# Optimization experiments

Hardware: AMD Instinct MI355X
Metric: run time of the kernel (lower is better)

## Reference

```python
import jax, jax.numpy as jnp
import numpy as np

B, S, E, H = 4, 2048, 1024, 16
DK = E // H  # 64


def setup_inputs() -> dict:
    key = jax.random.key(0)
    ks = jax.random.split(key, 6)
    scale = 1.0 / np.sqrt(E)
    return {
        "x": jax.random.normal(ks[0], (B, S, E), dtype=jnp.float32),
        "Wq": jax.random.normal(ks[1], (E, E), dtype=jnp.float32) * scale,
        "Wk": jax.random.normal(ks[2], (E, E), dtype=jnp.float32) * scale,
        "Wv": jax.random.normal(ks[3], (E, E), dtype=jnp.float32) * scale,
        "Wo": jax.random.normal(ks[4], (E, E), dtype=jnp.float32) * scale,
        "theta": jax.random.normal(ks[5], (DK,), dtype=jnp.float32),
    }


def _heads(t):
    # [B,S,E] -> [B,H,S,DK]
    b, s, _ = t.shape
    return t.reshape(b, s, H, DK).transpose(0, 2, 1, 3)


def reference(x, Wq, Wk, Wv, Wo, theta):
    # nn.Linear (no bias): y = x @ W.T
    # quantum transform: independent single-qubit RX(x)->RX(theta)->  <Z> = cos(x+theta)
    q = jnp.cos(_heads(x @ Wq.T) + theta)  # [B,H,S,DK]
    k = jnp.cos(_heads(x @ Wk.T) + theta)
    v = jnp.cos(_heads(x @ Wv.T) + theta)
    scores = jnp.einsum("bhqd,bhkd->bhqk", q, k) / jnp.sqrt(jnp.float32(DK))
    attn = jax.nn.softmax(scores, axis=-1)  # dropout is identity in eval
    out = jnp.einsum("bhqk,bhkd->bhqd", attn, v)  # [B,H,S,DK]
    out = out.transpose(0, 2, 1, 3).reshape(x.shape[0], -1, E)
    return out @ Wo.T
```

## Files before the change

### kernel.cpp

```cpp
#include <hip/hip_runtime.h>

#define B_  4
#define S_  2048
#define E_  1024
#define H_  16
#define DK_ 64
#define M_  (B_*S_)

typedef __attribute__((ext_vector_type(8)))  short short8;
typedef __attribute__((ext_vector_type(4)))  float f32x4;
typedef __attribute__((ext_vector_type(16))) float f32x16;

#define QSCALE 0.18033688f

__device__ __forceinline__ unsigned short f2b(float f) {
    union { float f; unsigned u; } v; v.f = f;
    unsigned u = v.u;
    return (unsigned short)((u + 0x7fffu + ((u >> 16) & 1u)) >> 16);
}

__device__ __forceinline__ void gload_lds16(const unsigned short* g, unsigned short* l) {
    __builtin_amdgcn_global_load_lds((const __attribute__((address_space(1))) void*)g,
                                     (__attribute__((address_space(3))) void*)l, 16, 0, 0);
}

__global__ __launch_bounds__(256) void cvt_x(const float* __restrict__ src,
                                             unsigned short* __restrict__ dst) {
    int i = blockIdx.x * 256 + threadIdx.x;
    float4 f = ((const float4*)src)[i];
    ushort4 o;
    o.x = f2b(f.x); o.y = f2b(f.y); o.z = f2b(f.z); o.w = f2b(f.w);
    ((ushort4*)dst)[i] = o;
}

__global__ __launch_bounds__(256) void cvt_w(const float* __restrict__ w0, const float* __restrict__ w1,
                                             const float* __restrict__ w2, const float* __restrict__ w3,
                                             unsigned short* __restrict__ wb,
                                             unsigned short* __restrict__ wob) {
    int z = blockIdx.y;
    const float* src = (z == 0) ? w0 : (z == 1) ? w1 : (z == 2) ? w2 : w3;
    unsigned short* dst = (z < 3) ? wb + (size_t)z * E_ * E_ : wob;
    int i = blockIdx.x * 256 + threadIdx.x;
    float4 f = ((const float4*)src)[i];
    ushort4 o;
    o.x = f2b(f.x); o.y = f2b(f.y); o.z = f2b(f.z); o.w = f2b(f.w);
    ((ushort4*)dst)[i] = o;
}

__global__ __launch_bounds__(256) void gemm_qkv(
    const unsigned short* __restrict__ xb,
    const unsigned short* __restrict__ Wb,
    const float* __restrict__ theta,
    unsigned short* __restrict__ qb,
    unsigned short* __restrict__ kb,
    unsigned short* __restrict__ vtb)
{
    __shared__ unsigned short smem[128*144];
    unsigned short* As = smem;
    unsigned short* Bs = smem + 128*64;
    const int tid = threadIdx.x;
    const int w = tid >> 6, lane = tid & 63, quad = lane >> 4, col = lane & 15;
    const int wm = (w & 1) * 64, wn = (w >> 1) * 64;
    const int m0 = blockIdx.x * 128, n0 = blockIdx.y * 128, z = blockIdx.z;
    const unsigned short* Wz = Wb + (size_t)z * E_ * E_;
    const int srow = lane >> 3, schunk = (lane & 7) * 8;

    f32x4 acc[4][4] = {};
    for (int k0 = 0; k0 < E_; k0 += 64) {
        #pragma unroll
        for (int c = 0; c < 4; c++) {
            int row = w*32 + c*8 + srow;
            gload_lds16(&xb[(size_t)(m0+row)*E_ + k0 + schunk], &As[(w*32 + c*8)*64]);
            gload_lds16(&Wz[(size_t)(n0+row)*E_ + k0 + schunk], &Bs[(w*32 + c*8)*64]);
        }
        __syncthreads();
        #pragma unroll
        for (int kk = 0; kk < 64; kk += 32) {
            short8 a[4], b[4];
            #pragma unroll
            for (int i = 0; i < 4; i++)
                a[i] = *(const short8*)&As[(wm + i*16 + col)*64 + kk + quad*8];
            #pragma unroll
            for (int j = 0; j < 4; j++)
                b[j] = *(const short8*)&Bs[(wn + j*16 + col)*64 + kk + quad*8];
            #pragma unroll
            for (int i = 0; i < 4; i++)
                #pragma unroll
                for (int j = 0; j < 4; j++)
                    acc[i][j] = __builtin_amdgcn_mfma_f32_16x16x32_bf16(a[i], b[j], acc[i][j], 0, 0, 0);
        }
        __syncthreads();
    }

    const int bblk = m0 >> 11;
    const int sbase = m0 & (S_-1);

    if (z != 2) {
        const float qs = (z == 0) ? QSCALE : 1.0f;
        #pragma unroll
        for (int j = 0; j < 4; j++) {
            int nl = wn + j*16 + col;
            float th = theta[(n0 + nl) & 63];
            #pragma unroll
            for (int i = 0; i < 4; i++)
                #pragma unroll
                for (int r = 0; r < 4; r++) {
                    int ml = wm + i*16 + quad*4 + r;
                    int nls = nl ^ (((ml >> 2) & 3) << 4);
                    smem[ml*144 + nls] = f2b(__cosf(acc[i][j][r] + th) * qs);
                }
        }
        __syncthreads();
        unsigned short* dst = (z == 0) ? qb : kb;
        const int h0 = n0 >> 6;
        #pragma unroll
        for (int k = 0; k < 8; k++) {
            int idx = k*256 + tid;
            int chunk = idx & 7, seg = idx >> 3;
            int ml = seg >> 1, hh = seg & 1;
            int ch = chunk ^ (((ml >> 2) & 3) << 1);
            int4 val = *(const int4*)&smem[ml*144 + hh*64 + ch*8];
            size_t g = ((size_t)(bblk*H_ + h0 + hh)*S_ + sbase + ml)*DK_ + chunk*8;
            *(int4*)&dst[g] = val;
        }
    } else {
        #pragma unroll
        for (int j = 0; j < 4; j++) {
            int nl = wn + j*16 + col;
            float th = theta[(n0 + nl) & 63];
            #pragma unroll
            for (int i = 0; i < 4; i++)
                #pragma unroll
                for (int r = 0; r < 4; r++)
                    smem[nl*136 + wm + i*16 + quad*4 + r] = f2b(__cosf(acc[i][j][r] + th));
        }
        __syncthreads();
        int row = tid >> 1, halfm = (tid & 1) * 64;
        int n = n0 + row, h = n >> 6, d = n & 63;
        size_t base = ((size_t)(bblk*H_ + h)*DK_ + d)*S_ + sbase + halfm;
        #pragma unroll
        for (int k = 0; k < 8; k++)
            *(int4*)&vtb[base + k*8] = *(const int4*)&smem[row*136 + halfm + k*8];
    }
}

__global__ __launch_bounds__(256) void gemm_out(
    const unsigned short* __restrict__ ctx,
    const unsigned short* __restrict__ Wob,
    float* __restrict__ out)
{
    __shared__ unsigned short As[128*64];
    __shared__ unsigned short Bs[128*64];
    const int tid = threadIdx.x;
    const int w = tid >> 6, lane = tid & 63, quad = lane >> 4, col = lane & 15;
    const int wm = (w & 1) * 64, wn = (w >> 1) * 64;
    const int m0 = blockIdx.x * 128, n0 = blockIdx.y * 128;
    const int srow = lane >> 3, schunk = (lane & 7) * 8;

    f32x4 acc[4][4] = {};
    for (int k0 = 0; k0 < E_; k0 += 64) {
        #pragma unroll
        for (int c = 0; c < 4; c++) {
            int row = w*32 + c*8 + srow;
            gload_lds16(&ctx[(size_t)(m0+row)*E_ + k0 + schunk], &As[(w*32 + c*8)*64]);
            gload_lds16(&Wob[(size_t)(n0+row)*E_ + k0 + schunk], &Bs[(w*32 + c*8)*64]);
        }
        __syncthreads();
        #pragma unroll
        for (int kk = 0; kk < 64; kk += 32) {
            short8 a[4], b[4];
            #pragma unroll
            for (int i = 0; i < 4; i++)
                a[i] = *(const short8*)&As[(wm + i*16 + col)*64 + kk + quad*8];
            #pragma unroll
            for (int j = 0; j < 4; j++)
                b[j] = *(const short8*)&Bs[(wn + j*16 + col)*64 + kk + quad*8];
            #pragma unroll
            for (int i = 0; i < 4; i++)
                #pragma unroll
                for (int j = 0; j < 4; j++)
                    acc[i][j] = __builtin_amdgcn_mfma_f32_16x16x32_bf16(a[i], b[j], acc[i][j], 0, 0, 0);
        }
        __syncthreads();
    }
    #pragma unroll
    for (int j = 0; j < 4; j++) {
        int n = n0 + wn + j*16 + col;
        #pragma unroll
        for (int i = 0; i < 4; i++)
            #pragma unroll
            for (int r = 0; r < 4; r++) {
                int m = m0 + wm + i*16 + quad*4 + r;
                out[(size_t)m*E_ + n] = acc[i][j][r];
            }
    }
}

#define LPK 72

__global__ __launch_bounds__(256, 4) void flash_attn(
    const unsigned short* __restrict__ qb,
    const unsigned short* __restrict__ kb,
    const unsigned short* __restrict__ vtb,
    unsigned short* __restrict__ ctx)
{
    __shared__ unsigned short Kt[64*LPK];
    __shared__ unsigned short Vt[64*LPK];
    const int tid = threadIdx.x;
    const int w = tid >> 6, lane = tid & 63, col = lane & 31, half = lane >> 5;
    const int q0 = blockIdx.x * 128;
    const int bh = blockIdx.y;

    short8 qf[4];
    {
        const unsigned short* qrow = qb + ((size_t)bh*S_ + q0 + w*32 + col)*DK_;
        #pragma unroll
        for (int c = 0; c < 4; c++)
            qf[c] = *(const short8*)&qrow[c*16 + half*8];
    }

    union U8 { unsigned u[4]; short8 s8; };
    U8 ones;
    #pragma unroll
    for (int i = 0; i < 4; i++) ones.u[i] = 0x3F803F80u;

    f32x16 oacc[2] = {};
    f32x16 lacc = {};

    for (int kt = 0; kt < S_; kt += 64) {
        __syncthreads();
        for (int i = tid; i < 512; i += 256) {
            int row = i >> 3, c8 = (i & 7) * 8;
            *(int4*)&Kt[row*LPK + c8] = *(const int4*)&kb [((size_t)bh*S_  + kt + row)*DK_ + c8];
            *(int4*)&Vt[row*LPK + c8] = *(const int4*)&vtb[((size_t)bh*DK_ + row)*S_ + kt + c8];
        }
        __syncthreads();

        #pragma unroll
        for (int t = 0; t < 2; t++) {
            f32x16 sacc = {};
            #pragma unroll
            for (int c = 0; c < 4; c++) {
                short8 kf = *(const short8*)&Kt[(t*32 + col)*LPK + c*16 + half*8];
                sacc = __builtin_amdgcn_mfma_f32_32x32x16_bf16(kf, qf[c], sacc, 0, 0, 0);
            }
            unsigned pk[4][2], pp[4][2];
            #pragma unroll
            for (int rg = 0; rg < 4; rg++) {
                float p0 = __builtin_amdgcn_exp2f(sacc[rg*4+0]);
                float p1 = __builtin_amdgcn_exp2f(sacc[rg*4+1]);
                float p2 = __builtin_amdgcn_exp2f(sacc[rg*4+2]);
                float p3 = __builtin_amdgcn_exp2f(sacc[rg*4+3]);
                pk[rg][0] = (__float_as_uint(p0) >> 16) | (__float_as_uint(p1) & 0xffff0000u);
                pk[rg][1] = (__float_as_uint(p2) >> 16) | (__float_as_uint(p3) & 0xffff0000u);
            }
            #pragma unroll
            for (int rg = 0; rg < 4; rg++) {
                pp[rg][0] = __shfl_xor((int)pk[rg][0], 32);
                pp[rg][1] = __shfl_xor((int)pk[rg][1], 32);
            }
            #pragma unroll
            for (int kc = 0; kc < 2; kc++) {
                const int lo = 2*kc, hi = 2*kc + 1;
                U8 pa;
                pa.u[0] = half ? pp[hi][0] : pk[lo][0];
                pa.u[1] = half ? pp[hi][1] : pk[lo][1];
                pa.u[2] = half ? pk[hi][0] : pp[lo][0];
                pa.u[3] = half ? pk[hi][1] : pp[lo][1];
                lacc = __builtin_amdgcn_mfma_f32_32x32x16_bf16(pa.s8, ones.s8, lacc, 0, 0, 0);
                #pragma unroll
                for (int dt = 0; dt < 2; dt++) {
                    short8 vf = *(const short8*)&Vt[(dt*32 + col)*LPK + t*32 + kc*16 + half*8];
                    oacc[dt] = __builtin_amdgcn_mfma_f32_32x32x16_bf16(pa.s8, vf, oacc[dt], 0, 0, 0);
                }
            }
        }
    }

    const int b = bh >> 4, h = bh & 15;
    #pragma unroll
    for (int rg = 0; rg < 4; rg++)
        #pragma unroll
        for (int rr = 0; rr < 4; rr++) {
            int row = rr + rg*8 + half*4;
            float inv = 1.0f / lacc[rg*4 + rr];
            int s = q0 + w*32 + row;
            size_t rowoff = ((size_t)(b*S_ + s))*E_ + h*64;
            #pragma unroll
            for (int dt = 0; dt < 2; dt++)
                ctx[rowoff + dt*32 + col] = f2b(oacc[dt][rg*4 + rr] * inv);
        }
}

extern "C" void kernel_launch(void* const* d_in, const int* in_sizes, int n_in,
                              void* d_out, int out_size, void* d_ws, size_t ws_size,
                              hipStream_t stream) {
    (void)in_sizes; (void)n_in; (void)out_size; (void)ws_size;
    const float* x     = (const float*)d_in[0];
    const float* Wq    = (const float*)d_in[1];
    const float* Wk    = (const float*)d_in[2];
    const float* Wv    = (const float*)d_in[3];
    const float* Wo    = (const float*)d_in[4];
    const float* theta = (const float*)d_in[5];
    float* out = (float*)d_out;

    unsigned short* ws  = (unsigned short*)d_ws;
    unsigned short* xb  = ws;
    unsigned short* Wb  = xb  + (size_t)M_*E_;
    unsigned short* Wob = Wb  + (size_t)3*E_*E_;
    unsigned short* qb  = Wob + (size_t)E_*E_;
    unsigned short* kb  = qb  + (size_t)B_*H_*S_*DK_;
    unsigned short* vtb = kb  + (size_t)B_*H_*S_*DK_;
    unsigned short* ctx = xb;

    cvt_x<<<M_*E_/4/256, 256, 0, stream>>>(x, xb);
    cvt_w<<<dim3(E_*E_/4/256, 4), 256, 0, stream>>>(Wq, Wk, Wv, Wo, Wb, Wob);

    gemm_qkv<<<dim3(M_/128, E_/128, 3), 256, 0, stream>>>(xb, Wb, theta, qb, kb, vtb);
    flash_attn<<<dim3(S_/128, B_*H_), 256, 0, stream>>>(qb, kb, vtb, ctx);
    gemm_out<<<dim3(M_/128, E_/128), 256, 0, stream>>>(ctx, Wob, out);
}
```

Measured before the change: 295.7 us.

## Double query rows per attention wave and replace row-sum MFMA with VALU sums

Each attention wave now handles two 32-row query groups, reusing the K and V fragments loaded from LDS across both groups and halving the number of blocks. The softmax denominator is accumulated with plain adds and a cross-half shuffle instead of an extra MFMA against a ones matrix, and bf16 packing uses byte-permute with fewer shuffles. The separate x and weight conversion kernels are merged into a single launch. In exchange, register pressure rises, the occupancy hint drops from 4 to 2 blocks, and fewer blocks are available to fill the GPU.

```diff
diff --git a/kernel.cpp b/kernel.cpp
--- a/kernel.cpp
+++ b/kernel.cpp
@@ -24,27 +24,30 @@
                                      (__attribute__((address_space(3))) void*)l, 16, 0, 0);
 }
 
-__global__ __launch_bounds__(256) void cvt_x(const float* __restrict__ src,
-                                             unsigned short* __restrict__ dst) {
+#define XN4 (M_*E_/4)
+#define WN4 (E_*E_/4)
+__global__ __launch_bounds__(256) void cvt_all(
+    const float* __restrict__ x,
+    const float* __restrict__ w0, const float* __restrict__ w1,
+    const float* __restrict__ w2, const float* __restrict__ w3,
+    unsigned short* __restrict__ xb, unsigned short* __restrict__ wb,
+    unsigned short* __restrict__ wob) {
     int i = blockIdx.x * 256 + threadIdx.x;
-    float4 f = ((const float4*)src)[i];
+    const float* src;
+    unsigned short* dst;
+    int idx;
+    if (i < XN4) { src = x; dst = xb; idx = i; }
+    else {
+        int j = i - XN4;
+        int z = j >> 18;
+        idx = j & (WN4 - 1);
+        src = (z == 0) ? w0 : (z == 1) ? w1 : (z == 2) ? w2 : w3;
+        dst = (z < 3) ? wb + (size_t)z * E_ * E_ : wob;
+    }
+    float4 f = ((const float4*)src)[idx];
     ushort4 o;
     o.x = f2b(f.x); o.y = f2b(f.y); o.z = f2b(f.z); o.w = f2b(f.w);
-    ((ushort4*)dst)[i] = o;
-}
-
-__global__ __launch_bounds__(256) void cvt_w(const float* __restrict__ w0, const float* __restrict__ w1,
-                                             const float* __restrict__ w2, const float* __restrict__ w3,
-                                             unsigned short* __restrict__ wb,
-                                             unsigned short* __restrict__ wob) {
-    int z = blockIdx.y;
-    const float* src = (z == 0) ? w0 : (z == 1) ? w1 : (z == 2) ? w2 : w3;
-    unsigned short* dst = (z < 3) ? wb + (size_t)z * E_ * E_ : wob;
-    int i = blockIdx.x * 256 + threadIdx.x;
-    float4 f = ((const float4*)src)[i];
-    ushort4 o;
-    o.x = f2b(f.x); o.y = f2b(f.y); o.z = f2b(f.z); o.w = f2b(f.w);
-    ((ushort4*)dst)[i] = o;
+    ((ushort4*)dst)[idx] = o;
 }
 
 __global__ __launch_bounds__(256) void gemm_qkv(
@@ -198,7 +201,7 @@
 
 #define LPK 72
 
-__global__ __launch_bounds__(256, 4) void flash_attn(
+__global__ __launch_bounds__(256, 2) void flash_attn(
     const unsigned short* __restrict__ qb,
     const unsigned short* __restrict__ kb,
     const unsigned short* __restrict__ vtb,
@@ -208,24 +211,22 @@
     __shared__ unsigned short Vt[64*LPK];
     const int tid = threadIdx.x;
     const int w = tid >> 6, lane = tid & 63, col = lane & 31, half = lane >> 5;
-    const int q0 = blockIdx.x * 128;
+    const int q0 = blockIdx.x * 256;
     const int bh = blockIdx.y;
 
-    short8 qf[4];
-    {
-        const unsigned short* qrow = qb + ((size_t)bh*S_ + q0 + w*32 + col)*DK_;
+    union U8 { unsigned u[4]; short8 s8; };
+
+    short8 qf[2][4];
+    #pragma unroll
+    for (int qg = 0; qg < 2; qg++) {
+        const unsigned short* qrow = qb + ((size_t)bh*S_ + q0 + w*64 + qg*32 + col)*DK_;
         #pragma unroll
         for (int c = 0; c < 4; c++)
-            qf[c] = *(const short8*)&qrow[c*16 + half*8];
-    }
-
-    union U8 { unsigned u[4]; short8 s8; };
-    U8 ones;
-    #pragma unroll
-    for (int i = 0; i < 4; i++) ones.u[i] = 0x3F803F80u;
-
-    f32x16 oacc[2] = {};
-    f32x16 lacc = {};
+            qf[qg][c] = *(const short8*)&qrow[c*16 + half*8];
+    }
+
+    float rsum[2] = {0.f, 0.f};
+    f32x16 oacc[2][2] = {};
 
     for (int kt = 0; kt < S_; kt += 64) {
         __syncthreads();
@@ -238,40 +239,49 @@
 
         #pragma unroll
         for (int t = 0; t < 2; t++) {
-            f32x16 sacc = {};
-            #pragma unroll
-            for (int c = 0; c < 4; c++) {
-                short8 kf = *(const short8*)&Kt[(t*32 + col)*LPK + c*16 + half*8];
-                sacc = __builtin_amdgcn_mfma_f32_32x32x16_bf16(kf, qf[c], sacc, 0, 0, 0);
-            }
-            unsigned pk[4][2], pp[4][2];
-            #pragma unroll
-            for (int rg = 0; rg < 4; rg++) {
-                float p0 = __builtin_amdgcn_exp2f(sacc[rg*4+0]);
-                float p1 = __builtin_amdgcn_exp2f(sacc[rg*4+1]);
-                float p2 = __builtin_amdgcn_exp2f(sacc[rg*4+2]);
-                float p3 = __builtin_amdgcn_exp2f(sacc[rg*4+3]);
-                pk[rg][0] = (__float_as_uint(p0) >> 16) | (__float_as_uint(p1) & 0xffff0000u);
-                pk[rg][1] = (__float_as_uint(p2) >> 16) | (__float_as_uint(p3) & 0xffff0000u);
-            }
-            #pragma unroll
-            for (int rg = 0; rg < 4; rg++) {
-                pp[rg][0] = __shfl_xor((int)pk[rg][0], 32);
-                pp[rg][1] = __shfl_xor((int)pk[rg][1], 32);
-            }
-            #pragma unroll
-            for (int kc = 0; kc < 2; kc++) {
-                const int lo = 2*kc, hi = 2*kc + 1;
-                U8 pa;
-                pa.u[0] = half ? pp[hi][0] : pk[lo][0];
-                pa.u[1] = half ? pp[hi][1] : pk[lo][1];
-                pa.u[2] = half ? pk[hi][0] : pp[lo][0];
-                pa.u[3] = half ? pk[hi][1] : pp[lo][1];
-                lacc = __builtin_amdgcn_mfma_f32_32x32x16_bf16(pa.s8, ones.s8, lacc, 0, 0, 0);
-                #pragma unroll
-                for (int dt = 0; dt < 2; dt++) {
-                    short8 vf = *(const short8*)&Vt[(dt*32 + col)*LPK + t*32 + kc*16 + half*8];
-                    oacc[dt] = __builtin_amdgcn_mfma_f32_32x32x16_bf16(pa.s8, vf, oacc[dt], 0, 0, 0);
+            short8 kf[4];
+            #pragma unroll
+            for (int c = 0; c < 4; c++)
+                kf[c] = *(const short8*)&Kt[(t*32 + col)*LPK + c*16 + half*8];
+            short8 vf[2][2];
+            #pragma unroll
+            for (int kc = 0; kc < 2; kc++)
+                #pragma unroll
+                for (int dt = 0; dt < 2; dt++)
+                    vf[kc][dt] = *(const short8*)&Vt[(dt*32 + col)*LPK + t*32 + kc*16 + half*8];
+
+            #pragma unroll
+            for (int qg = 0; qg < 2; qg++) {
+                f32x16 sacc = {};
+                #pragma unroll
+                for (int c = 0; c < 4; c++)
+                    sacc = __builtin_amdgcn_mfma_f32_32x32x16_bf16(kf[c], qf[qg][c], sacc, 0, 0, 0);
+                unsigned pk[4][2];
+                #pragma unroll
+                for (int rg = 0; rg < 4; rg++) {
+                    float p0 = __builtin_amdgcn_exp2f(sacc[rg*4+0]);
+                    float p1 = __builtin_amdgcn_exp2f(sacc[rg*4+1]);
+                    float p2 = __builtin_amdgcn_exp2f(sacc[rg*4+2]);
+                    float p3 = __builtin_amdgcn_exp2f(sacc[rg*4+3]);
+                    rsum[qg] += (p0 + p1) + (p2 + p3);
+                    pk[rg][0] = __builtin_amdgcn_perm(__float_as_uint(p1), __float_as_uint(p0), 0x07060302u);
+                    pk[rg][1] = __builtin_amdgcn_perm(__float_as_uint(p3), __float_as_uint(p2), 0x07060302u);
+                }
+                #pragma unroll
+                for (int kc = 0; kc < 2; kc++) {
+                    const int lo = 2*kc, hi = 2*kc + 1;
+                    unsigned t0 = half ? pk[lo][0] : pk[hi][0];
+                    unsigned t1 = half ? pk[lo][1] : pk[hi][1];
+                    unsigned r0 = __shfl_xor((int)t0, 32);
+                    unsigned r1 = __shfl_xor((int)t1, 32);
+                    U8 pa;
+                    pa.u[0] = half ? r0 : pk[lo][0];
+                    pa.u[1] = half ? r1 : pk[lo][1];
+                    pa.u[2] = half ? pk[hi][0] : r0;
+                    pa.u[3] = half ? pk[hi][1] : r1;
+                    #pragma unroll
+                    for (int dt = 0; dt < 2; dt++)
+                        oacc[qg][dt] = __builtin_amdgcn_mfma_f32_32x32x16_bf16(pa.s8, vf[kc][dt], oacc[qg][dt], 0, 0, 0);
                 }
             }
         }
@@ -279,17 +289,22 @@
 
     const int b = bh >> 4, h = bh & 15;
     #pragma unroll
-    for (int rg = 0; rg < 4; rg++)
-        #pragma unroll
-        for (int rr = 0; rr < 4; rr++) {
-            int row = rr + rg*8 + half*4;
-            float inv = 1.0f / lacc[rg*4 + rr];
-            int s = q0 + w*32 + row;
-            size_t rowoff = ((size_t)(b*S_ + s))*E_ + h*64;
-            #pragma unroll
-            for (int dt = 0; dt < 2; dt++)
-                ctx[rowoff + dt*32 + col] = f2b(oacc[dt][rg*4 + rr] * inv);
-        }
+    for (int qg = 0; qg < 2; qg++) {
+        float l = rsum[qg] + __shfl_xor(rsum[qg], 32);
+        float inv = 1.0f / l;
+        #pragma unroll
+        for (int rg = 0; rg < 4; rg++)
+            #pragma unroll
+            for (int rr = 0; rr < 4; rr++) {
+                int row = rr + rg*8 + half*4;
+                float invr = __shfl(inv, row);
+                int s = q0 + w*64 + qg*32 + row;
+                size_t rowoff = ((size_t)(b*S_ + s))*E_ + h*64;
+                #pragma unroll
+                for (int dt = 0; dt < 2; dt++)
+                    ctx[rowoff + dt*32 + col] = f2b(oacc[qg][dt][rg*4 + rr] * invr);
+            }
+    }
 }
 
 extern "C" void kernel_launch(void* const* d_in, const int* in_sizes, int n_in,
@@ -313,10 +328,9 @@
     unsigned short* vtb = kb  + (size_t)B_*H_*S_*DK_;
     unsigned short* ctx = xb;
 
-    cvt_x<<<M_*E_/4/256, 256, 0, stream>>>(x, xb);
-    cvt_w<<<dim3(E_*E_/4/256, 4), 256, 0, stream>>>(Wq, Wk, Wv, Wo, Wb, Wob);
+    cvt_all<<<(XN4 + 4*WN4)/256, 256, 0, stream>>>(x, Wq, Wk, Wv, Wo, xb, Wb, Wob);
 
     gemm_qkv<<<dim3(M_/128, E_/128, 3), 256, 0, stream>>>(xb, Wb, theta, qb, kb, vtb);
-    flash_attn<<<dim3(S_/128, B_*H_), 256, 0, stream>>>(qb, kb, vtb, ctx);
+    flash_attn<<<dim3(S_/256, B_*H_), 256, 0, stream>>>(qb, kb, vtb, ctx);
     gemm_out<<<dim3(M_/128, E_/128), 256, 0, stream>>>(ctx, Wob, out);
 }
```

New measurement: 298.7 us. No clear change (+1.0%).
